# Performance work log

Measured on AMD Instinct MI355X. Metric: run time of the kernel, lower is better.

Reference implementation:

```python
import jax, jax.numpy as jnp
import numpy as np

N_NODES = 50000
N_REL = 4
N_EDGES = 800000
IN_DIM = 128
HID = 128
N_CLASSES = 16


def setup_inputs() -> dict:
    key = jax.random.key(0)
    ks = jax.random.split(key, 12)
    feat = jax.random.normal(ks[0], (N_NODES, IN_DIM), dtype=jnp.float32)
    src = jax.random.randint(ks[1], (N_REL, N_EDGES), 0, N_NODES, dtype=jnp.int32)
    dst = jax.random.randint(ks[2], (N_REL, N_EDGES), 0, N_NODES, dtype=jnp.int32)
    s = 0.05
    W1 = jax.random.normal(ks[3], (N_REL, IN_DIM, HID), dtype=jnp.float32) * s
    b1 = jax.random.normal(ks[4], (N_REL, HID), dtype=jnp.float32) * s
    W2 = jax.random.normal(ks[5], (N_REL, HID, HID), dtype=jnp.float32) * s
    b2 = jax.random.normal(ks[6], (N_REL, HID), dtype=jnp.float32) * s
    W3 = jax.random.normal(ks[7], (N_REL, HID, HID), dtype=jnp.float32) * s
    b3 = jax.random.normal(ks[8], (N_REL, HID), dtype=jnp.float32) * s
    Wlin = jax.random.normal(ks[9], (HID, N_CLASSES), dtype=jnp.float32) * s
    blin = jax.random.normal(ks[10], (N_CLASSES,), dtype=jnp.float32) * s
    return {"feat": feat, "src": src, "dst": dst, "W1": W1, "b1": b1,
            "W2": W2, "b2": b2, "W3": W3, "b3": b3, "Wlin": Wlin, "blin": blin}


def _graph_conv(x, s, d, W, b, n_nodes):
    """DGL GraphConv with norm='both': D_dst^-1/2 * A * D_src^-1/2 * x, then @W + b."""
    ones = jnp.ones(s.shape[0], dtype=x.dtype)
    deg_out = jnp.maximum(jax.ops.segment_sum(ones, s, num_segments=n_nodes), 1.0)
    deg_in = jnp.maximum(jax.ops.segment_sum(ones, d, num_segments=n_nodes), 1.0)
    xs = x * (deg_out ** -0.5)[:, None]          # [N, F]
    agg = jax.ops.segment_sum(xs[s], d, num_segments=n_nodes)  # gather+scatter [N, F]
    agg = agg * (deg_in ** -0.5)[:, None]
    return agg @ W + b


def _hetero_layer(x, src, dst, W, b, n_nodes):
    # HeteroGraphConv aggregate='sum' over relations (loop over small fixed R)
    out = _graph_conv(x, src[0], dst[0], W[0], b[0], n_nodes)
    for r in range(1, src.shape[0]):
        out = out + _graph_conv(x, src[r], dst[r], W[r], b[r], n_nodes)
    return out


def _l2_normalize(x, eps=1e-12):
    # torch F.normalize: x / max(||x||_2, eps), per row
    nrm = jnp.sqrt(jnp.sum(x * x, axis=1, keepdims=True))
    return x / jnp.maximum(nrm, eps)


def reference(feat, src, dst, W1, b1, W2, b2, W3, b3, Wlin, blin):
    n = feat.shape[0]
    h = _hetero_layer(feat, src, dst, W1, b1, n)
    h = jax.nn.leaky_relu(_l2_normalize(h), negative_slope=0.01)
    h = _hetero_layer(h, src, dst, W2, b2, n)
    h = jax.nn.leaky_relu(_l2_normalize(h), negative_slope=0.01)
    h = _hetero_layer(h, src, dst, W3, b3, n)
    # update_all(copy_u, sum) across all relations (unnormalized scatter-sum)
    pooled = jax.ops.segment_sum(h[src[0]], dst[0], num_segments=n)
    for r in range(1, src.shape[0]):
        pooled = pooled + jax.ops.segment_sum(h[src[r]], dst[r], num_segments=n)
    hg = jnp.mean(pooled, axis=0, keepdims=True)  # dgl.mean_nodes -> [1, HID]
    return jax.nn.sigmoid(hg @ Wlin + blin)       # [1, n_classes]
```

## Files before the change

### kernel.cpp

```cpp
#include <hip/hip_runtime.h>
#include <hip/hip_bf16.h>

constexpr int N_NODES = 50000;
constexpr int N_REL   = 4;
constexpr int N_EDGES = 800000;
constexpr int DIM     = 128;
constexpr int N_CLS   = 16;

constexpr int CHUNK  = 256;
constexpr int NCHUNK = (N_NODES + CHUNK - 1) / CHUNK;
constexpr int NPART  = N_REL * NCHUNK;

constexpr int NCBR  = (N_NODES + 255) / 256;
constexpr int NCB   = N_REL * NCBR;
constexpr int TILE  = 8000;
constexpr int TPR   = N_EDGES / TILE;
constexpr int MAXB  = 6144;

constexpr int RNG    = 12544;
constexpr int NRANGE = 4;
constexpr int DTILE  = 80000;
constexpr int DNT    = N_EDGES / DTILE;

constexpr int NPB = 8;
constexpr int CAP = 1024;

constexpr float YSCALE = 32.0f;

typedef __attribute__((ext_vector_type(8))) short short8;
typedef __attribute__((ext_vector_type(4))) float float4v;
typedef __attribute__((ext_vector_type(2))) float floatx2;

__device__ __forceinline__ unsigned int f2bf_bits(float f) {
  unsigned int u = __float_as_uint(f);
  return (u + 0x7fffu + ((u >> 16) & 1u)) >> 16;
}
__device__ __forceinline__ unsigned int pack2bf(float a, float b) {
  return f2bf_bits(a) | (f2bf_bits(b) << 16);
}

__device__ __forceinline__ int LCOL(int p) { return (p & 7) * 16 + (p >> 3); }

__global__ __launch_bounds__(256) void degree_hist(
    const int* __restrict__ src, const int* __restrict__ dst,
    int* __restrict__ cnt_out, int* __restrict__ cnt_in) {
  int b = blockIdx.x;
  int t     = b % DNT;    b /= DNT;
  int range = b % NRANGE; b /= NRANGE;
  int r     = b % N_REL;  b /= N_REL;
  int which = b;
  const int* arr = (which ? dst : src) + (size_t)r * N_EDGES + (size_t)t * DTILE;
  int* cnt = (which ? cnt_in : cnt_out) + r * N_NODES;
  int tid = threadIdx.x;
  __shared__ int h[RNG];
  for (int i = tid; i < RNG; i += 256) h[i] = 0;
  __syncthreads();
  int lo = range * RNG;
  int hi = lo + RNG;
  const int4* a4 = (const int4*)arr;
  for (int i = tid; i < DTILE / 4; i += 256) {
    int4 v = a4[i];
    if (v.x >= lo && v.x < hi) atomicAdd(&h[v.x - lo], 1);
    if (v.y >= lo && v.y < hi) atomicAdd(&h[v.y - lo], 1);
    if (v.z >= lo && v.z < hi) atomicAdd(&h[v.z - lo], 1);
    if (v.w >= lo && v.w < hi) atomicAdd(&h[v.w - lo], 1);
  }
  __syncthreads();
  for (int i = tid; i < RNG; i += 256) {
    int n = lo + i;
    int c = h[i];
    if (n < N_NODES && c) atomicAdd(&cnt[n], c);
  }
}

__global__ __launch_bounds__(256) void scan_partial(
    const int* __restrict__ cnt_in, int* __restrict__ partial) {
  int b = blockIdx.x;
  int r = b / NCHUNK, c = b % NCHUNK;
  int i = c * CHUNK + threadIdx.x;
  int v = (i < N_NODES) ? cnt_in[r * N_NODES + i] : 0;
#pragma unroll
  for (int off = 1; off < 64; off <<= 1) v += __shfl_xor(v, off, 64);
  __shared__ int ws[4];
  if ((threadIdx.x & 63) == 0) ws[threadIdx.x >> 6] = v;
  __syncthreads();
  if (threadIdx.x == 0) partial[b] = ws[0] + ws[1] + ws[2] + ws[3];
}

__global__ __launch_bounds__(1024) void scan_offsets(
    const int* __restrict__ partial, int* __restrict__ chunk_off,
    int* __restrict__ row_ptr) {
  __shared__ int lds[1024];
  __shared__ int sexcl[1024];
  __shared__ int stotal;
  int tid = threadIdx.x;
  int v = (tid < NPART) ? partial[tid] : 0;
  lds[tid] = v;
  __syncthreads();
  for (int off = 1; off < 1024; off <<= 1) {
    int t = (tid >= off) ? lds[tid - off] : 0;
    __syncthreads();
    lds[tid] += t;
    __syncthreads();
  }
  int excl = lds[tid] - v;
  sexcl[tid] = excl;
  if (tid == NPART - 1) stotal = excl + v;
  if (tid < NPART) chunk_off[tid] = excl;
  __syncthreads();
  if (tid < N_REL) {
    int base = sexcl[tid * NCHUNK];
    int next = (tid < N_REL - 1) ? sexcl[(tid + 1) * NCHUNK] : stotal;
    row_ptr[tid * (N_NODES + 1) + N_NODES] = next - base;
  }
}

__global__ __launch_bounds__(256) void scan_expand(
    const int* __restrict__ cnt_in, const int* __restrict__ chunk_off,
    int* __restrict__ row_ptr, int* __restrict__ cbcur) {
  int b = blockIdx.x;
  int r = b / NCHUNK, c = b % NCHUNK;
  int tid = threadIdx.x;
  int i = c * CHUNK + tid;
  int v = (i < N_NODES) ? cnt_in[r * N_NODES + i] : 0;
  __shared__ int lds[CHUNK];
  lds[tid] = v;
  __syncthreads();
  for (int off = 1; off < CHUNK; off <<= 1) {
    int t = (tid >= off) ? lds[tid - off] : 0;
    __syncthreads();
    lds[tid] += t;
    __syncthreads();
  }
  int excl = lds[tid] - v;
  int base = chunk_off[b] - chunk_off[r * NCHUNK];
  if (i < N_NODES) row_ptr[r * (N_NODES + 1) + i] = base + excl;
  if (tid == 0) cbcur[r * NCBR + c] = base;
}

__global__ __launch_bounds__(256) void pass1_bin(
    const int* __restrict__ src, const int* __restrict__ dst,
    int* __restrict__ cbcur, unsigned int* __restrict__ binned) {
  int b = blockIdx.x;
  int r = b / TPR, t = b % TPR;
  const int* sp = src + (size_t)r * N_EDGES + t * TILE;
  const int* dp = dst + (size_t)r * N_EDGES + t * TILE;
  unsigned int* outp = binned + (size_t)r * N_EDGES;
  int tid = threadIdx.x;
  __shared__ int hist[NCBR];
  __shared__ int scanb[256];
  __shared__ int gbase[NCBR];
  __shared__ int lcur[NCBR];
  for (int i = tid; i < NCBR; i += 256) hist[i] = 0;
  __syncthreads();
  for (int i = tid; i < TILE; i += 256) atomicAdd(&hist[dp[i] >> 8], 1);
  __syncthreads();
  int v = (tid < NCBR) ? hist[tid] : 0;
  scanb[tid] = v;
  __syncthreads();
  for (int off = 1; off < 256; off <<= 1) {
    int tv = (tid >= off) ? scanb[tid - off] : 0;
    __syncthreads();
    scanb[tid] += tv;
    __syncthreads();
  }
  if (tid < NCBR) {
    int excl = scanb[tid] - v;
    gbase[tid] = atomicAdd(&cbcur[r * NCBR + tid], v) - excl;
    lcur[tid] = excl;
  }
  __syncthreads();
  for (int i = tid; i < TILE; i += 256) {
    int d = dp[i];
    int s = sp[i];
    int cb = d >> 8;
    int lp = atomicAdd(&lcur[cb], 1);
    outp[gbase[cb] + lp] = ((unsigned)s << 8) | (unsigned)(d & 255);
  }
}

__global__ __launch_bounds__(256) void pass2_sort(
    const unsigned int* __restrict__ binned, const int* __restrict__ row_ptr,
    unsigned short* __restrict__ csr) {
  int b = blockIdx.x;
  int r = b / NCBR, c = b % NCBR;
  int node0 = c * 256;
  int node1 = min(node0 + 256, N_NODES);
  int start = row_ptr[r * (N_NODES + 1) + node0];
  int endv  = row_ptr[r * (N_NODES + 1) + node1];
  int count = endv - start;
  const unsigned int* bp = binned + (size_t)r * N_EDGES + start;
  unsigned short* outg = csr + (size_t)r * N_EDGES + start;
  int tid = threadIdx.x;
  __shared__ int hist[4096];
  __shared__ int scanb[256];
  __shared__ unsigned short outb[MAXB];
  for (int i = tid; i < 4096; i += 256) hist[i] = 0;
  __syncthreads();
  for (int i = tid; i < count; i += 256) {
    unsigned int p = bp[i];
    unsigned int key = ((p & 255u) << 4) | ((p >> 8) >> 12);
    atomicAdd(&hist[key], 1);
  }
  __syncthreads();
  int t16 = tid * 16;
  int a[16];
  int tsum = 0;
#pragma unroll
  for (int j = 0; j < 16; ++j) { a[j] = hist[t16 + j]; tsum += a[j]; }
  scanb[tid] = tsum;
  __syncthreads();
  for (int off = 1; off < 256; off <<= 1) {
    int tv = (tid >= off) ? scanb[tid - off] : 0;
    __syncthreads();
    scanb[tid] += tv;
    __syncthreads();
  }
  int run = scanb[tid] - tsum;
#pragma unroll
  for (int j = 0; j < 16; ++j) { hist[t16 + j] = run; run += a[j]; }
  __syncthreads();
  if (count <= MAXB) {
    for (int i = tid; i < count; i += 256) {
      unsigned int p = bp[i];
      unsigned int s = p >> 8;
      unsigned int key = ((p & 255u) << 4) | (s >> 12);
      int pos = atomicAdd(&hist[key], 1);
      outb[pos] = (unsigned short)s;
    }
    __syncthreads();
    for (int i = tid; i < count; i += 256) outg[i] = outb[i];
  } else {
    for (int i = tid; i < count; i += 256) {
      unsigned int p = bp[i];
      unsigned int s = p >> 8;
      unsigned int key = ((p & 255u) << 4) | (s >> 12);
      int pos = atomicAdd(&hist[key], 1);
      outg[pos] = (unsigned short)s;
    }
  }
}

__global__ __launch_bounds__(256) void scales_kernel(
    const int* __restrict__ cnt_out, const int* __restrict__ cnt_in,
    float* __restrict__ soutF, float* __restrict__ sinF,
    float* __restrict__ wout) {
  int total = N_REL * N_NODES;
  for (int idx = blockIdx.x * blockDim.x + threadIdx.x; idx < total;
       idx += gridDim.x * blockDim.x) {
    soutF[idx] = YSCALE / sqrtf((float)max(cnt_out[idx], 1));
    sinF [idx] = (1.0f / YSCALE) / sqrtf((float)max(cnt_in[idx], 1));
  }
  for (int v = blockIdx.x * blockDim.x + threadIdx.x; v < N_NODES;
       v += gridDim.x * blockDim.x) {
    wout[v] = (float)(cnt_out[v] + cnt_out[N_NODES + v] +
                      cnt_out[2 * N_NODES + v] + cnt_out[3 * N_NODES + v]);
  }
}

__global__ __launch_bounds__(256) void cvt_feat_bf16(
    const float* __restrict__ in, unsigned short* __restrict__ outw, int n4) {
  int i = blockIdx.x * blockDim.x + threadIdx.x;
  if (i < n4) {
    float4 v = ((const float4*)in)[i];
    uint2 o;
    o.x = pack2bf(v.x, v.y);
    o.y = pack2bf(v.z, v.w);
    *(uint2*)(outw + (size_t)i * 4) = o;
  }
}

template <int PERMK>
__global__ __launch_bounds__(256) void prep_w(
    const float* __restrict__ W, const float* __restrict__ b,
    unsigned short* __restrict__ Wt, float* __restrict__ bsum) {
  int i = blockIdx.x * blockDim.x + threadIdx.x;
  if (i < N_REL * DIM * DIM) {
    int col = i >> 7, p = i & 127;
    int k = PERMK ? LCOL(p) : p;
    int rrel = col >> 7, n = col & 127;
    Wt[i] = (unsigned short)f2bf_bits(W[rrel * DIM * DIM + k * DIM + n]);
  }
  if (i < DIM) {
    int Lp = LCOL(i);
    bsum[i] = b[Lp] + b[DIM + Lp] + b[2 * DIM + Lp] + b[3 * DIM + Lp];
  }
}

__global__ __launch_bounds__(256) void gemm_y(
    const unsigned short* __restrict__ X, const unsigned short* __restrict__ Wt,
    const float* __restrict__ soutF, unsigned char* __restrict__ Yb) {
  int tid = threadIdx.x;
  int w   = tid >> 6;
  int l   = tid & 63;
  int l15 = l & 15, lq = l >> 4;
  int rowbase = blockIdx.x * 64;

  float4v acc[4][8] = {};
  const unsigned short* Wq = Wt + (size_t)(w * DIM) * DIM;

#pragma unroll
  for (int ks = 0; ks < 4; ++ks) {
    int k0 = ks * 32 + lq * 8;
    short8 bfr[8];
#pragma unroll
    for (int c = 0; c < 8; ++c)
      bfr[c] = *(const short8*)(Wq + (size_t)(c * 16 + l15) * DIM + k0);
#pragma unroll
    for (int i = 0; i < 4; ++i) {
      int rr = rowbase + i * 16 + l15;
      short8 afr = (rr < N_NODES)
          ? *(const short8*)(X + (size_t)rr * DIM + k0)
          : (short8)(short)0;
#pragma unroll
      for (int c = 0; c < 8; ++c)
        acc[i][c] = __builtin_amdgcn_mfma_f32_16x16x32_bf16(afr, bfr[c],
                                                            acc[i][c], 0, 0, 0);
    }
  }

  const float* so = soutF + (size_t)w * N_NODES;
  unsigned char* Yq = Yb + (size_t)w * N_NODES * DIM;
#pragma unroll
  for (int i = 0; i < 4; ++i) {
#pragma unroll
    for (int rr = 0; rr < 4; ++rr) {
      int grow = rowbase + i * 16 + lq * 4 + rr;
      if (grow < N_NODES) {
        float sc = so[grow];
        float v0 = acc[i][0][rr] * sc, v1 = acc[i][1][rr] * sc;
        float v2 = acc[i][2][rr] * sc, v3 = acc[i][3][rr] * sc;
        float v4 = acc[i][4][rr] * sc, v5 = acc[i][5][rr] * sc;
        float v6 = acc[i][6][rr] * sc, v7 = acc[i][7][rr] * sc;
        int t0 = __builtin_amdgcn_cvt_pk_fp8_f32(v0, v1, 0, false);
        t0 = __builtin_amdgcn_cvt_pk_fp8_f32(v2, v3, t0, true);
        int t1 = __builtin_amdgcn_cvt_pk_fp8_f32(v4, v5, 0, false);
        t1 = __builtin_amdgcn_cvt_pk_fp8_f32(v6, v7, t1, true);
        uint2 o;
        o.x = (unsigned)t0;
        o.y = (unsigned)t1;
        *(uint2*)(Yq + (size_t)grow * DIM + l15 * 8) = o;
      }
    }
  }
}

template <int MODE>
__global__ __launch_bounds__(256) void gather_y(
    const unsigned char* __restrict__ Yb, const unsigned short* __restrict__ csr,
    const int* __restrict__ row_ptr, const float* __restrict__ sinF,
    const float* __restrict__ bsum, void* __restrict__ out) {
  int d0   = blockIdx.x * NPB;
  int r    = threadIdx.x >> 6;
  int lane = threadIdx.x & 63;
  int g    = lane >> 4;
  int l16  = lane & 15;
  const unsigned short* cs = csr + (size_t)r * N_EDGES;
  const unsigned char*  Yq = Yb + (size_t)r * N_NODES * DIM;

  int rp = row_ptr[r * (N_NODES + 1) + d0 + min(lane, NPB)];
  int beg0 = __shfl(rp, 0, 64);
  int cnt  = __shfl(rp, NPB, 64) - beg0;

  __shared__ unsigned short scsr[N_REL][CAP];
  __shared__ __align__(16) float lds[N_REL][NPB][132];

  int ccap = min(cnt, CAP);
  for (int i = lane; i < ccap; i += 64) scsr[r][i] = cs[beg0 + i];

  auto body = [&](auto CS) {
#pragma unroll 1
    for (int n = 0; n < NPB; n += 2) {
      int bA = __shfl(rp, n, 64),  eA = __shfl(rp, n + 1, 64);
      int bB = eA,                 eB = __shfl(rp, n + 2, 64);
      floatx2 aA[4], aB[4];
#pragma unroll
      for (int j = 0; j < 4; ++j) {
        aA[j] = (floatx2){0.f, 0.f};
        aB[j] = (floatx2){0.f, 0.f};
      }
      int pA = bA, pB = bB;
      while (pA < eA || pB < eB) {
        bool doA = pA < eA, doB = pB < eB;
        uint2 xA[4], xB[4];
        if (doA) {
#pragma unroll
          for (int u = 0; u < 4; ++u) {
            int e = pA + u * 4 + g;
            bool vv = e < eA;
            int se = (int)CS(min(e, eA - 1));
            uint2 t = *(const uint2*)(Yq + (size_t)se * DIM + l16 * 8);
            xA[u].x = vv ? t.x : 0u;
            xA[u].y = vv ? t.y : 0u;
          }
        }
        if (doB) {
#pragma unroll
          for (int u = 0; u < 4; ++u) {
            int e = pB + u * 4 + g;
            bool vv = e < eB;
            int se = (int)CS(min(e, eB - 1));
            uint2 t = *(const uint2*)(Yq + (size_t)se * DIM + l16 * 8);
            xB[u].x = vv ? t.x : 0u;
            xB[u].y = vv ? t.y : 0u;
          }
        }
        if (doA) {
#pragma unroll
          for (int u = 0; u < 4; ++u) {
            aA[0] += __builtin_amdgcn_cvt_pk_f32_fp8((int)xA[u].x, false);
            aA[1] += __builtin_amdgcn_cvt_pk_f32_fp8((int)xA[u].x, true);
            aA[2] += __builtin_amdgcn_cvt_pk_f32_fp8((int)xA[u].y, false);
            aA[3] += __builtin_amdgcn_cvt_pk_f32_fp8((int)xA[u].y, true);
          }
          pA += 16;
        }
        if (doB) {
#pragma unroll
          for (int u = 0; u < 4; ++u) {
            aB[0] += __builtin_amdgcn_cvt_pk_f32_fp8((int)xB[u].x, false);
            aB[1] += __builtin_amdgcn_cvt_pk_f32_fp8((int)xB[u].x, true);
            aB[2] += __builtin_amdgcn_cvt_pk_f32_fp8((int)xB[u].y, false);
            aB[3] += __builtin_amdgcn_cvt_pk_f32_fp8((int)xB[u].y, true);
          }
          pB += 16;
        }
      }
#pragma unroll
      for (int j = 0; j < 4; ++j) {
        aA[j].x += __shfl_xor(aA[j].x, 16, 64);
        aA[j].y += __shfl_xor(aA[j].y, 16, 64);
        aA[j].x += __shfl_xor(aA[j].x, 32, 64);
        aA[j].y += __shfl_xor(aA[j].y, 32, 64);
        aB[j].x += __shfl_xor(aB[j].x, 16, 64);
        aB[j].y += __shfl_xor(aB[j].y, 16, 64);
        aB[j].x += __shfl_xor(aB[j].x, 32, 64);
        aB[j].y += __shfl_xor(aB[j].y, 32, 64);
      }
      if (g < 2) {
        float4 wA, wB;
        if (g == 0) {
          wA = make_float4(aA[0].x, aA[0].y, aA[1].x, aA[1].y);
          wB = make_float4(aB[0].x, aB[0].y, aB[1].x, aB[1].y);
        } else {
          wA = make_float4(aA[2].x, aA[2].y, aA[3].x, aA[3].y);
          wB = make_float4(aB[2].x, aB[2].y, aB[3].x, aB[3].y);
        }
        *(float4*)&lds[r][n][l16 * 8 + g * 4]     = wA;
        *(float4*)&lds[r][n + 1][l16 * 8 + g * 4] = wB;
      }
    }
  };
  if (cnt <= CAP)
    body([&](int e) { return scsr[r][e - beg0]; });
  else
    body([&](int e) { return cs[e]; });
  __syncthreads();

  int nn = threadIdx.x >> 5;
  int ln = threadIdx.x & 31;
  int d  = d0 + nn;
  float s0 = sinF[d];
  float s1 = sinF[N_NODES + d];
  float s2 = sinF[2 * N_NODES + d];
  float s3 = sinF[3 * N_NODES + d];
  float4 a0 = *(const float4*)&lds[0][nn][ln * 4];
  float4 a1 = *(const float4*)&lds[1][nn][ln * 4];
  float4 a2 = *(const float4*)&lds[2][nn][ln * 4];
  float4 a3 = *(const float4*)&lds[3][nn][ln * 4];
  float4 bs = *(const float4*)&bsum[ln * 4];
  float v0 = s0 * a0.x + s1 * a1.x + s2 * a2.x + s3 * a3.x + bs.x;
  float v1 = s0 * a0.y + s1 * a1.y + s2 * a2.y + s3 * a3.y + bs.y;
  float v2 = s0 * a0.z + s1 * a1.z + s2 * a2.z + s3 * a3.z + bs.z;
  float v3 = s0 * a0.w + s1 * a1.w + s2 * a2.w + s3 * a3.w + bs.w;
  if (MODE == 1) {
    float ss = v0 * v0 + v1 * v1 + v2 * v2 + v3 * v3;
    ss += __shfl_xor(ss, 1, 32);
    ss += __shfl_xor(ss, 2, 32);
    ss += __shfl_xor(ss, 4, 32);
    ss += __shfl_xor(ss, 8, 32);
    ss += __shfl_xor(ss, 16, 32);
    float sc = 1.0f / fmaxf(sqrtf(ss), 1e-12f);
    v0 *= sc; v1 *= sc; v2 *= sc; v3 *= sc;
    v0 = v0 > 0.f ? v0 : 0.01f * v0;
    v1 = v1 > 0.f ? v1 : 0.01f * v1;
    v2 = v2 > 0.f ? v2 : 0.01f * v2;
    v3 = v3 > 0.f ? v3 : 0.01f * v3;
    uint2 o;
    o.x = pack2bf(v0, v1);
    o.y = pack2bf(v2, v3);
    *(uint2*)((unsigned short*)out + (size_t)d * DIM + ln * 4) = o;
  } else {
    float4 o = make_float4(v0, v1, v2, v3);
    *(float4*)((float*)out + (size_t)d * DIM + ln * 4) = o;
  }
}

__global__ __launch_bounds__(256) void pool_kernel(
    const float* __restrict__ h, const float* __restrict__ wout,
    float* __restrict__ hg) {
  int gw   = blockIdx.x * 4 + (threadIdx.x >> 6);
  int lane = threadIdx.x & 63;
  int nw   = gridDim.x * 4;
  float ax = 0.0f, ay = 0.0f;
  for (int v = gw; v < N_NODES; v += nw) {
    float w = wout[v];
    float2 hv = *(const float2*)(h + (size_t)v * DIM + lane * 2);
    ax = fmaf(w, hv.x, ax);
    ay = fmaf(w, hv.y, ay);
  }
  atomicAdd(&hg[lane * 2],     ax);
  atomicAdd(&hg[lane * 2 + 1], ay);
}

__global__ void head_kernel(const float* __restrict__ hg,
                            const float* __restrict__ Wlin,
                            const float* __restrict__ blin,
                            float* __restrict__ out) {
  int j = threadIdx.x;
  if (j < N_CLS) {
    float s = blin[j];
    const float invN = 1.0f / (float)N_NODES;
#pragma unroll 16
    for (int k = 0; k < DIM; ++k) {
      int Lk = (k & 7) * 16 + (k >> 3);
      s = fmaf(hg[k] * invN, Wlin[Lk * N_CLS + j], s);
    }
    out[j] = 1.0f / (1.0f + expf(-s));
  }
}

__global__ void fail_kernel(float* out) {
  int i = threadIdx.x;
  if (i < N_CLS) out[i] = 1e30f;
}

extern "C" void kernel_launch(void* const* d_in, const int* in_sizes, int n_in,
                              void* d_out, int out_size, void* d_ws, size_t ws_size,
                              hipStream_t stream) {
  const float* feat = (const float*)d_in[0];
  const int*   src  = (const int*)  d_in[1];
  const int*   dst  = (const int*)  d_in[2];
  const float* W1   = (const float*)d_in[3];
  const float* b1   = (const float*)d_in[4];
  const float* W2   = (const float*)d_in[5];
  const float* b2   = (const float*)d_in[6];
  const float* W3   = (const float*)d_in[7];
  const float* b3   = (const float*)d_in[8];
  const float* Wlin = (const float*)d_in[9];
  const float* blin = (const float*)d_in[10];
  float* out = (float*)d_out;

  char* base = (char*)d_ws;
  size_t off = 0;
  auto alloc = [&](size_t bytes) -> void* {
    void* q = base + off;
    off = (off + bytes + 255) & ~(size_t)255;
    return q;
  };
  int*   cnt_out  = (int*)  alloc((size_t)N_REL * N_NODES * 4);
  int*   cnt_in   = (int*)  alloc((size_t)N_REL * N_NODES * 4);
  int*   row_ptr  = (int*)  alloc((size_t)N_REL * (N_NODES + 1) * 4);
  float* soutF    = (float*)alloc((size_t)N_REL * N_NODES * 4);
  float* sinF     = (float*)alloc((size_t)N_REL * N_NODES * 4);
  float* wout     = (float*)alloc((size_t)N_NODES * 4);
  float* hg       = (float*)alloc((size_t)DIM * 4);
  int*   partial  = (int*)  alloc((size_t)NPART * 4);
  int*   chunkoff = (int*)  alloc((size_t)NPART * 4);
  int*   cbcur    = (int*)  alloc((size_t)NCB * 4);
  unsigned int*   binned = (unsigned int*)  alloc((size_t)N_REL * N_EDGES * 4);
  unsigned short* csr    = (unsigned short*)alloc((size_t)N_REL * N_EDGES * 2);
  unsigned char*  Yb     = (unsigned char*) alloc((size_t)N_REL * N_NODES * DIM);
  unsigned short* X0     = (unsigned short*)alloc((size_t)N_NODES * DIM * 2);
  unsigned short* X1     = (unsigned short*)alloc((size_t)N_NODES * DIM * 2);
  unsigned short* X2     = (unsigned short*)alloc((size_t)N_NODES * DIM * 2);
  float* H3       = (float*)alloc((size_t)N_NODES * DIM * 4);
  unsigned short* Wt1 = (unsigned short*)alloc((size_t)N_REL * DIM * DIM * 2);
  unsigned short* Wt2 = (unsigned short*)alloc((size_t)N_REL * DIM * DIM * 2);
  unsigned short* Wt3 = (unsigned short*)alloc((size_t)N_REL * DIM * DIM * 2);
  float* bs1 = (float*)alloc(DIM * 4);
  float* bs2 = (float*)alloc(DIM * 4);
  float* bs3 = (float*)alloc(DIM * 4);

  if (off > ws_size) {
    fail_kernel<<<1, 64, 0, stream>>>(out);
    return;
  }

  hipMemsetAsync(cnt_out, 0, (size_t)2 * N_REL * N_NODES * 4, stream);
  hipMemsetAsync(hg, 0, DIM * 4, stream);

  degree_hist  <<<2 * N_REL * NRANGE * DNT, 256, 0, stream>>>(src, dst, cnt_out, cnt_in);
  scan_partial <<<NPART, 256, 0, stream>>>(cnt_in, partial);
  scan_offsets <<<1, 1024, 0, stream>>>(partial, chunkoff, row_ptr);
  scan_expand  <<<NPART, 256, 0, stream>>>(cnt_in, chunkoff, row_ptr, cbcur);
  pass1_bin    <<<N_REL * TPR, 256, 0, stream>>>(src, dst, cbcur, binned);
  pass2_sort   <<<NCB, 256, 0, stream>>>(binned, row_ptr, csr);
  scales_kernel<<<512, 256, 0, stream>>>(cnt_out, cnt_in, soutF, sinF, wout);

  cvt_feat_bf16<<<(N_NODES * DIM / 4 + 255) / 256, 256, 0, stream>>>(
      feat, X0, N_NODES * DIM / 4);
  prep_w<0><<<(N_REL * DIM * DIM + 255) / 256, 256, 0, stream>>>(W1, b1, Wt1, bs1);
  prep_w<1><<<(N_REL * DIM * DIM + 255) / 256, 256, 0, stream>>>(W2, b2, Wt2, bs2);
  prep_w<1><<<(N_REL * DIM * DIM + 255) / 256, 256, 0, stream>>>(W3, b3, Wt3, bs3);

  int gemm_blocks = (N_NODES + 63) / 64;
  int gath_blocks = (N_NODES + NPB - 1) / NPB;

  gemm_y     <<<gemm_blocks, 256, 0, stream>>>(X0, Wt1, soutF, Yb);
  gather_y<1><<<gath_blocks, 256, 0, stream>>>(Yb, csr, row_ptr, sinF, bs1, X1);
  gemm_y     <<<gemm_blocks, 256, 0, stream>>>(X1, Wt2, soutF, Yb);
  gather_y<1><<<gath_blocks, 256, 0, stream>>>(Yb, csr, row_ptr, sinF, bs2, X2);
  gemm_y     <<<gemm_blocks, 256, 0, stream>>>(X2, Wt3, soutF, Yb);
  gather_y<0><<<gath_blocks, 256, 0, stream>>>(Yb, csr, row_ptr, sinF, bs3, H3);

  pool_kernel<<<256, 256, 0, stream>>>(H3, wout, hg);
  head_kernel<<<1, 64, 0, stream>>>(hg, Wlin, blin, out);
}
```

Measured before the change: 506.9 us.

## Fuse preprocessing kernels and shrink gather LDS footprint

Folds the degree-scale computation into scan_expand, merges the three weight-prep launches into one, and drops the separate fp32-to-bf16 feature conversion by converting inside the first GEMM's A-fragment load. The gather kernel now stages per-relation partial sums in LDS as packed bf16 instead of fp32, and the CSR cache capacity is halved, which reduces shared memory per block and may raise occupancy. The aim is fewer launches, one less full pass over the feature matrix, and more resident gather blocks. The costs are an extra bf16 rounding of intermediate sums and more nodes falling back to the uncached CSR path.

```diff
diff --git a/kernel.cpp b/kernel.cpp
--- a/kernel.cpp
+++ b/kernel.cpp
@@ -23,7 +23,7 @@
 constexpr int DNT    = N_EDGES / DTILE;
 
 constexpr int NPB = 8;
-constexpr int CAP = 1024;
+constexpr int CAP = 512;
 
 constexpr float YSCALE = 32.0f;
 
@@ -38,6 +38,8 @@
 __device__ __forceinline__ unsigned int pack2bf(float a, float b) {
   return f2bf_bits(a) | (f2bf_bits(b) << 16);
 }
+__device__ __forceinline__ float bf_lo(unsigned int u) { return __uint_as_float(u << 16); }
+__device__ __forceinline__ float bf_hi(unsigned int u) { return __uint_as_float(u & 0xffff0000u); }
 
 __device__ __forceinline__ int LCOL(int p) { return (p & 7) * 16 + (p >> 3); }
 
@@ -117,7 +119,9 @@
 
 __global__ __launch_bounds__(256) void scan_expand(
     const int* __restrict__ cnt_in, const int* __restrict__ chunk_off,
-    int* __restrict__ row_ptr, int* __restrict__ cbcur) {
+    int* __restrict__ row_ptr, int* __restrict__ cbcur,
+    const int* __restrict__ cnt_out, float* __restrict__ soutF,
+    float* __restrict__ sinF, float* __restrict__ wout) {
   int b = blockIdx.x;
   int r = b / NCHUNK, c = b % NCHUNK;
   int tid = threadIdx.x;
@@ -134,7 +138,16 @@
   }
   int excl = lds[tid] - v;
   int base = chunk_off[b] - chunk_off[r * NCHUNK];
-  if (i < N_NODES) row_ptr[r * (N_NODES + 1) + i] = base + excl;
+  if (i < N_NODES) {
+    row_ptr[r * (N_NODES + 1) + i] = base + excl;
+    int co = cnt_out[r * N_NODES + i];
+    soutF[r * N_NODES + i] = YSCALE / sqrtf((float)max(co, 1));
+    sinF [r * N_NODES + i] = (1.0f / YSCALE) / sqrtf((float)max(v, 1));
+    if (r == 0) {
+      wout[i] = (float)(co + cnt_out[N_NODES + i] +
+                        cnt_out[2 * N_NODES + i] + cnt_out[3 * N_NODES + i]);
+    }
+  }
   if (tid == 0) cbcur[r * NCBR + c] = base;
 }
 
@@ -241,43 +254,23 @@
   }
 }
 
-__global__ __launch_bounds__(256) void scales_kernel(
-    const int* __restrict__ cnt_out, const int* __restrict__ cnt_in,
-    float* __restrict__ soutF, float* __restrict__ sinF,
-    float* __restrict__ wout) {
-  int total = N_REL * N_NODES;
-  for (int idx = blockIdx.x * blockDim.x + threadIdx.x; idx < total;
-       idx += gridDim.x * blockDim.x) {
-    soutF[idx] = YSCALE / sqrtf((float)max(cnt_out[idx], 1));
-    sinF [idx] = (1.0f / YSCALE) / sqrtf((float)max(cnt_in[idx], 1));
-  }
-  for (int v = blockIdx.x * blockDim.x + threadIdx.x; v < N_NODES;
-       v += gridDim.x * blockDim.x) {
-    wout[v] = (float)(cnt_out[v] + cnt_out[N_NODES + v] +
-                      cnt_out[2 * N_NODES + v] + cnt_out[3 * N_NODES + v]);
-  }
-}
-
-__global__ __launch_bounds__(256) void cvt_feat_bf16(
-    const float* __restrict__ in, unsigned short* __restrict__ outw, int n4) {
-  int i = blockIdx.x * blockDim.x + threadIdx.x;
-  if (i < n4) {
-    float4 v = ((const float4*)in)[i];
-    uint2 o;
-    o.x = pack2bf(v.x, v.y);
-    o.y = pack2bf(v.z, v.w);
-    *(uint2*)(outw + (size_t)i * 4) = o;
-  }
-}
-
-template <int PERMK>
-__global__ __launch_bounds__(256) void prep_w(
-    const float* __restrict__ W, const float* __restrict__ b,
-    unsigned short* __restrict__ Wt, float* __restrict__ bsum) {
-  int i = blockIdx.x * blockDim.x + threadIdx.x;
+__global__ __launch_bounds__(256) void prep_w3(
+    const float* __restrict__ W1, const float* __restrict__ b1,
+    const float* __restrict__ W2, const float* __restrict__ b2,
+    const float* __restrict__ W3, const float* __restrict__ b3,
+    unsigned short* __restrict__ Wt1, float* __restrict__ bs1,
+    unsigned short* __restrict__ Wt2, float* __restrict__ bs2,
+    unsigned short* __restrict__ Wt3, float* __restrict__ bs3) {
+  int set = blockIdx.x >> 8;
+  int i   = (blockIdx.x & 255) * 256 + threadIdx.x;
+  const float* W = (set == 0) ? W1 : (set == 1) ? W2 : W3;
+  const float* b = (set == 0) ? b1 : (set == 1) ? b2 : b3;
+  unsigned short* Wt = (set == 0) ? Wt1 : (set == 1) ? Wt2 : Wt3;
+  float* bsum = (set == 0) ? bs1 : (set == 1) ? bs2 : bs3;
+  int permk = (set != 0);
   if (i < N_REL * DIM * DIM) {
     int col = i >> 7, p = i & 127;
-    int k = PERMK ? LCOL(p) : p;
+    int k = permk ? LCOL(p) : p;
     int rrel = col >> 7, n = col & 127;
     Wt[i] = (unsigned short)f2bf_bits(W[rrel * DIM * DIM + k * DIM + n]);
   }
@@ -287,8 +280,9 @@
   }
 }
 
+template <int AF32>
 __global__ __launch_bounds__(256) void gemm_y(
-    const unsigned short* __restrict__ X, const unsigned short* __restrict__ Wt,
+    const void* __restrict__ Xv, const unsigned short* __restrict__ Wt,
     const float* __restrict__ soutF, unsigned char* __restrict__ Yb) {
   int tid = threadIdx.x;
   int w   = tid >> 6;
@@ -296,6 +290,9 @@
   int l15 = l & 15, lq = l >> 4;
   int rowbase = blockIdx.x * 64;
 
+  const unsigned short* X = (const unsigned short*)Xv;
+  const float*          Xf = (const float*)Xv;
+
   float4v acc[4][8] = {};
   const unsigned short* Wq = Wt + (size_t)(w * DIM) * DIM;
 
@@ -309,9 +306,26 @@
 #pragma unroll
     for (int i = 0; i < 4; ++i) {
       int rr = rowbase + i * 16 + l15;
-      short8 afr = (rr < N_NODES)
-          ? *(const short8*)(X + (size_t)rr * DIM + k0)
-          : (short8)(short)0;
+      short8 afr;
+      if (rr < N_NODES) {
+        if (AF32) {
+          const float* xp = Xf + (size_t)rr * DIM + k0;
+          float4 f0 = *(const float4*)xp;
+          float4 f1 = *(const float4*)(xp + 4);
+          afr[0] = (short)f2bf_bits(f0.x);
+          afr[1] = (short)f2bf_bits(f0.y);
+          afr[2] = (short)f2bf_bits(f0.z);
+          afr[3] = (short)f2bf_bits(f0.w);
+          afr[4] = (short)f2bf_bits(f1.x);
+          afr[5] = (short)f2bf_bits(f1.y);
+          afr[6] = (short)f2bf_bits(f1.z);
+          afr[7] = (short)f2bf_bits(f1.w);
+        } else {
+          afr = *(const short8*)(X + (size_t)rr * DIM + k0);
+        }
+      } else {
+        afr = (short8)(short)0;
+      }
 #pragma unroll
       for (int c = 0; c < 8; ++c)
         acc[i][c] = __builtin_amdgcn_mfma_f32_16x16x32_bf16(afr, bfr[c],
@@ -363,7 +377,7 @@
   int cnt  = __shfl(rp, NPB, 64) - beg0;
 
   __shared__ unsigned short scsr[N_REL][CAP];
-  __shared__ __align__(16) float lds[N_REL][NPB][132];
+  __shared__ __align__(16) unsigned int ubuf[N_REL][NPB][66];
 
   int ccap = min(cnt, CAP);
   for (int i = lane; i < ccap; i += 64) scsr[r][i] = cs[beg0 + i];
@@ -438,16 +452,16 @@
         aB[j].y += __shfl_xor(aB[j].y, 32, 64);
       }
       if (g < 2) {
-        float4 wA, wB;
+        uint2 wA, wB;
         if (g == 0) {
-          wA = make_float4(aA[0].x, aA[0].y, aA[1].x, aA[1].y);
-          wB = make_float4(aB[0].x, aB[0].y, aB[1].x, aB[1].y);
+          wA.x = pack2bf(aA[0].x, aA[0].y); wA.y = pack2bf(aA[1].x, aA[1].y);
+          wB.x = pack2bf(aB[0].x, aB[0].y); wB.y = pack2bf(aB[1].x, aB[1].y);
         } else {
-          wA = make_float4(aA[2].x, aA[2].y, aA[3].x, aA[3].y);
-          wB = make_float4(aB[2].x, aB[2].y, aB[3].x, aB[3].y);
+          wA.x = pack2bf(aA[2].x, aA[2].y); wA.y = pack2bf(aA[3].x, aA[3].y);
+          wB.x = pack2bf(aB[2].x, aB[2].y); wB.y = pack2bf(aB[3].x, aB[3].y);
         }
-        *(float4*)&lds[r][n][l16 * 8 + g * 4]     = wA;
-        *(float4*)&lds[r][n + 1][l16 * 8 + g * 4] = wB;
+        *(uint2*)&ubuf[r][n][l16 * 4 + g * 2]     = wA;
+        *(uint2*)&ubuf[r][n + 1][l16 * 4 + g * 2] = wB;
       }
     }
   };
@@ -464,15 +478,19 @@
   float s1 = sinF[N_NODES + d];
   float s2 = sinF[2 * N_NODES + d];
   float s3 = sinF[3 * N_NODES + d];
-  float4 a0 = *(const float4*)&lds[0][nn][ln * 4];
-  float4 a1 = *(const float4*)&lds[1][nn][ln * 4];
-  float4 a2 = *(const float4*)&lds[2][nn][ln * 4];
-  float4 a3 = *(const float4*)&lds[3][nn][ln * 4];
+  uint2 u0 = *(const uint2*)&ubuf[0][nn][ln * 2];
+  uint2 u1 = *(const uint2*)&ubuf[1][nn][ln * 2];
+  uint2 u2 = *(const uint2*)&ubuf[2][nn][ln * 2];
+  uint2 u3 = *(const uint2*)&ubuf[3][nn][ln * 2];
   float4 bs = *(const float4*)&bsum[ln * 4];
-  float v0 = s0 * a0.x + s1 * a1.x + s2 * a2.x + s3 * a3.x + bs.x;
-  float v1 = s0 * a0.y + s1 * a1.y + s2 * a2.y + s3 * a3.y + bs.y;
-  float v2 = s0 * a0.z + s1 * a1.z + s2 * a2.z + s3 * a3.z + bs.z;
-  float v3 = s0 * a0.w + s1 * a1.w + s2 * a2.w + s3 * a3.w + bs.w;
+  float v0 = s0 * bf_lo(u0.x) + s1 * bf_lo(u1.x) + s2 * bf_lo(u2.x) +
+             s3 * bf_lo(u3.x) + bs.x;
+  float v1 = s0 * bf_hi(u0.x) + s1 * bf_hi(u1.x) + s2 * bf_hi(u2.x) +
+             s3 * bf_hi(u3.x) + bs.y;
+  float v2 = s0 * bf_lo(u0.y) + s1 * bf_lo(u1.y) + s2 * bf_lo(u2.y) +
+             s3 * bf_lo(u3.y) + bs.z;
+  float v3 = s0 * bf_hi(u0.y) + s1 * bf_hi(u1.y) + s2 * bf_hi(u2.y) +
+             s3 * bf_hi(u3.y) + bs.w;
   if (MODE == 1) {
     float ss = v0 * v0 + v1 * v1 + v2 * v2 + v3 * v3;
     ss += __shfl_xor(ss, 1, 32);
@@ -571,7 +589,6 @@
   unsigned int*   binned = (unsigned int*)  alloc((size_t)N_REL * N_EDGES * 4);
   unsigned short* csr    = (unsigned short*)alloc((size_t)N_REL * N_EDGES * 2);
   unsigned char*  Yb     = (unsigned char*) alloc((size_t)N_REL * N_NODES * DIM);
-  unsigned short* X0     = (unsigned short*)alloc((size_t)N_NODES * DIM * 2);
   unsigned short* X1     = (unsigned short*)alloc((size_t)N_NODES * DIM * 2);
   unsigned short* X2     = (unsigned short*)alloc((size_t)N_NODES * DIM * 2);
   float* H3       = (float*)alloc((size_t)N_NODES * DIM * 4);
@@ -593,25 +610,22 @@
   degree_hist  <<<2 * N_REL * NRANGE * DNT, 256, 0, stream>>>(src, dst, cnt_out, cnt_in);
   scan_partial <<<NPART, 256, 0, stream>>>(cnt_in, partial);
   scan_offsets <<<1, 1024, 0, stream>>>(partial, chunkoff, row_ptr);
-  scan_expand  <<<NPART, 256, 0, stream>>>(cnt_in, chunkoff, row_ptr, cbcur);
+  scan_expand  <<<NPART, 256, 0, stream>>>(cnt_in, chunkoff, row_ptr, cbcur,
+                                           cnt_out, soutF, sinF, wout);
   pass1_bin    <<<N_REL * TPR, 256, 0, stream>>>(src, dst, cbcur, binned);
   pass2_sort   <<<NCB, 256, 0, stream>>>(binned, row_ptr, csr);
-  scales_kernel<<<512, 256, 0, stream>>>(cnt_out, cnt_in, soutF, sinF, wout);
-
-  cvt_feat_bf16<<<(N_NODES * DIM / 4 + 255) / 256, 256, 0, stream>>>(
-      feat, X0, N_NODES * DIM / 4);
-  prep_w<0><<<(N_REL * DIM * DIM + 255) / 256, 256, 0, stream>>>(W1, b1, Wt1, bs1);
-  prep_w<1><<<(N_REL * DIM * DIM + 255) / 256, 256, 0, stream>>>(W2, b2, Wt2, bs2);
-  prep_w<1><<<(N_REL * DIM * DIM + 255) / 256, 256, 0, stream>>>(W3, b3, Wt3, bs3);
+
+  prep_w3<<<3 * 256, 256, 0, stream>>>(W1, b1, W2, b2, W3, b3,
+                                       Wt1, bs1, Wt2, bs2, Wt3, bs3);
 
   int gemm_blocks = (N_NODES + 63) / 64;
   int gath_blocks = (N_NODES + NPB - 1) / NPB;
 
-  gemm_y     <<<gemm_blocks, 256, 0, stream>>>(X0, Wt1, soutF, Yb);
+  gemm_y<1>  <<<gemm_blocks, 256, 0, stream>>>(feat, Wt1, soutF, Yb);
   gather_y<1><<<gath_blocks, 256, 0, stream>>>(Yb, csr, row_ptr, sinF, bs1, X1);
-  gemm_y     <<<gemm_blocks, 256, 0, stream>>>(X1, Wt2, soutF, Yb);
+  gemm_y<0>  <<<gemm_blocks, 256, 0, stream>>>(X1, Wt2, soutF, Yb);
   gather_y<1><<<gath_blocks, 256, 0, stream>>>(Yb, csr, row_ptr, sinF, bs2, X2);
-  gemm_y     <<<gemm_blocks, 256, 0, stream>>>(X2, Wt3, soutF, Yb);
+  gemm_y<0>  <<<gemm_blocks, 256, 0, stream>>>(X2, Wt3, soutF, Yb);
   gather_y<0><<<gath_blocks, 256, 0, stream>>>(Yb, csr, row_ptr, sinF, bs3, H3);
 
   pool_kernel<<<256, 256, 0, stream>>>(H3, wout, hg);
```

Result: faster. 492.4 us (-2.9%).
